# Optimization experiments

Measured on AMD Instinct MI355X. Metric: run time of the kernel, lower is better.

Reference implementation:

```python
import jax, jax.numpy as jnp
import numpy as np
import math

B, T, IN_DIM = 2, 2048, 512
D, NH, MULT, N_LAYER = 512, 8, 4, 3
N = D * MULT // NH  # per-head latent dim = 256
OUT_DIM = 512
THETA = 2 ** 16


def get_freqs(n):
    t = jnp.arange(n, dtype=jnp.float32)
    q = jnp.floor(t / 2.0) * 2.0  # quantize(q=2)
    return 1.0 / (THETA ** (q / n)) / (2.0 * math.pi)


def ln(x, eps=1e-5):
    mu = jnp.mean(x, axis=-1, keepdims=True)
    var = jnp.var(x, axis=-1, keepdims=True)
    return (x - mu) * jax.lax.rsqrt(var + eps)


def rope(phases, v):
    # phases: [T, N] broadcastable to v [B, nh, T, N]
    p = (phases % 1.0) * (2.0 * math.pi)
    pc, ps = jnp.cos(p), jnp.sin(p)
    # interleave rotate: out[..., 2i] = -v[..., 2i+1], out[..., 2i+1] = v[..., 2i]
    v_rot = jnp.stack((-v[..., 1::2], v[..., ::2]), axis=-1).reshape(v.shape)
    return v * pc + v_rot * ps


def setup_inputs() -> dict:
    key = jax.random.key(0)
    ks = jax.random.split(key, 8)
    std = 0.02
    return {
        "x": jax.random.normal(ks[0], (B, T, IN_DIM), dtype=jnp.float32),
        "w_in": jax.random.normal(ks[1], (IN_DIM, D), dtype=jnp.float32) * std,
        "b_in": jnp.zeros((D,), dtype=jnp.float32),
        "encoder": jax.random.normal(ks[2], (NH, D, N), dtype=jnp.float32) * std,
        "encoder_v": jax.random.normal(ks[3], (NH, D, N), dtype=jnp.float32) * std,
        "decoder": jax.random.normal(ks[4], (NH * N, D), dtype=jnp.float32) * std,
        "head_w": jax.random.normal(ks[5], (D, OUT_DIM), dtype=jnp.float32) * std,
        "head_b": jnp.zeros((OUT_DIM,), dtype=jnp.float32),
    }


def reference(x, w_in, b_in, encoder, encoder_v, decoder, head_w, head_b):
    freqs = get_freqs(N)  # [N]
    t_idx = jnp.arange(T, dtype=jnp.float32)
    phases = t_idx[:, None] * freqs[None, :]  # [T, N]
    # strict lower-triangular causal mask (tril diagonal=-1)
    mask = (jnp.arange(T)[:, None] > jnp.arange(T)[None, :])  # [T, T]
    dec = decoder.reshape(NH, N, D)

    xs = ln(x @ w_in + b_in)  # [B, T, D]
    for _ in range(N_LAYER):
        x_res = xs
        x_sparse = jax.nn.relu(jnp.einsum('btd,hdn->bhtn', xs, encoder))  # [B,nh,T,N]
        QR = rope(phases, x_sparse)
        scores = jnp.einsum('bhtn,bhsn->bhts', QR, QR)
        scores = jnp.where(mask, scores, 0.0)
        yKV = jnp.einsum('bhts,bsd->bhtd', scores, xs)  # V = x (head-broadcast)
        yKV = ln(yKV)
        y_sparse = jax.nn.relu(jnp.einsum('bhtd,hdn->bhtn', yKV, encoder_v))
        xy_sparse = x_sparse * y_sparse  # dropout p=0 -> identity
        yMLP = jnp.einsum('bhtn,hnd->btd', xy_sparse, dec)
        xs = ln(x_res + ln(yMLP))
    logits = xs @ head_w + head_b
    return logits
```

## Files before the change

### kernel.cpp

```cpp
#include <hip/hip_runtime.h>
#include <math.h>

constexpr int B_  = 2;
constexpr int T_  = 2048;
constexpr int D_  = 512;
constexpr int NH_ = 8;
constexpr int NL_ = 256;
constexpr int HN_ = NH_ * NL_;
constexpr int BT_ = B_ * T_;

typedef __bf16 v8bf __attribute__((ext_vector_type(8)));
typedef float  v4f  __attribute__((ext_vector_type(4)));
typedef unsigned short us8 __attribute__((ext_vector_type(8)));
typedef unsigned short us4 __attribute__((ext_vector_type(4)));

__device__ inline unsigned short f2b(float f) {
    union { float f; unsigned u; } v{f};
    unsigned r = v.u + 0x7FFF + ((v.u >> 16) & 1);
    return (unsigned short)(r >> 16);
}
__device__ inline float b2f(unsigned short u) {
    union { unsigned u; float f; } v{(unsigned)u << 16};
    return v.f;
}

__device__ __forceinline__ void g2l16(const void* g, void* l) {
    __builtin_amdgcn_global_load_lds(
        (const __attribute__((address_space(1))) void*)g,
        (__attribute__((address_space(3))) void*)l, 16, 0, 0);
}

#define TILE_IDS                                              \
    int tid = threadIdx.x;                                    \
    int lane = tid & 63, wid = tid >> 6;                      \
    int wm = (wid & 1) * 64, wn = (wid >> 1) * 64;            \
    int ln16 = lane & 15, q = lane >> 4;                      \
    int srl = lane >> 2, scl = (lane & 3) * 8;                \
    (void)wm; (void)wn;

#define T128_STAGE(Ab, lda, Bb, ldb, k0, buf)                 \
    _Pragma("unroll")                                         \
    for (int ci = 0; ci < 4; ++ci) {                          \
        int c = wid * 4 + ci;                                 \
        if (c < 8) {                                          \
            int r = c * 16 + srl;                             \
            g2l16(Ab + (long)r * lda + (k0) + scl,            \
                  (char*)As[buf] + c * 1024);                 \
        } else {                                              \
            int r = (c - 8) * 16 + srl;                       \
            g2l16(Bb + (long)r * ldb + (k0) + scl,            \
                  (char*)Bs[buf] + (c - 8) * 1024);           \
        }                                                     \
    }

#define TILE_MFMA(Asx, Bsx)                                   \
    {                                                         \
        v8bf af[4], bfr[4];                                   \
        _Pragma("unroll")                                     \
        for (int r = 0; r < 4; ++r)                           \
            af[r] = *(const v8bf*)&Asx[wm + r * 16 + ln16][q * 8]; \
        _Pragma("unroll")                                     \
        for (int c = 0; c < 4; ++c)                           \
            bfr[c] = *(const v8bf*)&Bsx[wn + c * 16 + ln16][q * 8]; \
        _Pragma("unroll")                                     \
        for (int r = 0; r < 4; ++r)                           \
            _Pragma("unroll")                                 \
            for (int c = 0; c < 4; ++c)                       \
                acc[r][c] = __builtin_amdgcn_mfma_f32_16x16x32_bf16( \
                    af[r], bfr[c], acc[r][c], 0, 0, 0);       \
    }

template <int KS, bool RELU, bool MUL, bool BF16OUT, bool LNA>
__global__ __launch_bounds__(256) void gemm128(
    const unsigned short* __restrict__ A, int lda, long sA,
    const unsigned short* __restrict__ Bt, int ldb, long sB,
    void* __restrict__ Cv, int ldc, long sC,
    const unsigned short* __restrict__ mulp, int K,
    const float* __restrict__ muinv, const float* __restrict__ colsum) {
    constexpr int NHF = KS / 32;
    int m0 = blockIdx.y * 128, n0 = blockIdx.x * 128, z = blockIdx.z;
    __shared__ unsigned short As[2][NHF][128][32];
    __shared__ unsigned short Bs[2][NHF][128][32];
    const unsigned short* Ab = A  + (long)z * sA + (long)m0 * lda;
    const unsigned short* Bb = Bt + (long)z * sB + (long)n0 * ldb;
    TILE_IDS
    v4f acc[4][4] = {};
    auto stageK = [&](int k0, int buf) {
        #pragma unroll
        for (int h = 0; h < NHF; ++h)
            #pragma unroll
            for (int ci = 0; ci < 4; ++ci) {
                int c = wid * 4 + ci;
                if (c < 8)
                    g2l16(Ab + (long)(c * 16 + srl) * lda + k0 + h * 32 + scl,
                          (char*)As[buf][h] + c * 1024);
                else
                    g2l16(Bb + (long)((c - 8) * 16 + srl) * ldb + k0 + h * 32 +
                              scl,
                          (char*)Bs[buf][h] + (c - 8) * 1024);
            }
    };
    stageK(0, 0);
    __syncthreads();
    int cur = 0;
    for (int k0 = 0; k0 < K; k0 += KS) {
        if (k0 + KS < K) stageK(k0 + KS, cur ^ 1);
        #pragma unroll
        for (int h = 0; h < NHF; ++h)
            TILE_MFMA(As[cur][h], Bs[cur][h])
        __syncthreads();
        cur ^= 1;
    }
    float* Cf = (float*)Cv;
    unsigned short* Cb = (unsigned short*)Cv;
    long zoff = (long)z * sC;
    #pragma unroll
    for (int r = 0; r < 4; ++r)
        #pragma unroll
        for (int c = 0; c < 4; ++c)
            #pragma unroll
            for (int e = 0; e < 4; ++e) {
                int row = m0 + wm + r * 16 + q * 4 + e;
                int col = n0 + wn + c * 16 + ln16;
                float v = acc[r][c][e];
                if (LNA) {
                    float2 mi = *(const float2*)&muinv[((long)z * BT_ + row) * 2];
                    float cs = colsum[(long)z * NL_ + col];
                    v = mi.y * (v - mi.x * cs);
                }
                if (RELU) v = fmaxf(v, 0.f);
                long idx = zoff + (long)row * ldc + col;
                if (MUL) v *= b2f(mulp[idx]);
                if (BF16OUT) Cb[idx] = f2b(v);
                else         Cf[idx] = v;
            }
}

__global__ __launch_bounds__(256) void enc_rope(
    const unsigned short* __restrict__ A,
    const unsigned short* __restrict__ Bt,
    unsigned short* __restrict__ xsp,
    unsigned short* __restrict__ qrh,
    unsigned short* __restrict__ qrT) {
    int m0 = blockIdx.y * 128, n0 = blockIdx.x * 128;
    __shared__ unsigned short As[2][2][128][32];
    __shared__ unsigned short Bs[2][2][128][32];
    unsigned short (*lt)[68] = (unsigned short(*)[68])&As[0][0][0][0];
    const unsigned short* Ab = A + (long)m0 * 512;
    const unsigned short* Bb = Bt + (long)n0 * 512;
    TILE_IDS
    v4f acc[4][4] = {};
    auto stageK = [&](int k0, int buf) {
        #pragma unroll
        for (int h = 0; h < 2; ++h)
            #pragma unroll
            for (int ci = 0; ci < 4; ++ci) {
                int c = wid * 4 + ci;
                if (c < 8)
                    g2l16(Ab + (long)(c * 16 + srl) * 512 + k0 + h * 32 + scl,
                          (char*)As[buf][h] + c * 1024);
                else
                    g2l16(Bb + (long)((c - 8) * 16 + srl) * 512 + k0 + h * 32 +
                              scl,
                          (char*)Bs[buf][h] + (c - 8) * 1024);
            }
    };
    stageK(0, 0);
    __syncthreads();
    int cur = 0;
    for (int k0 = 0; k0 < 512; k0 += 64) {
        if (k0 + 64 < 512) stageK(k0 + 64, cur ^ 1);
        TILE_MFMA(As[cur][0], Bs[cur][0])
        TILE_MFMA(As[cur][1], Bs[cur][1])
        __syncthreads();
        cur ^= 1;
    }
    int bb = m0 >> 11;
    int tbase = m0 & (T_ - 1);
    #pragma unroll
    for (int half = 0; half < 2; ++half) {
        if (wm == half * 64) {
            #pragma unroll
            for (int r = 0; r < 4; ++r)
                #pragma unroll
                for (int c = 0; c < 4; ++c)
                    #pragma unroll
                    for (int e = 0; e < 4; ++e) {
                        int rl = wm + r * 16 + q * 4 + e;
                        int col = n0 + wn + c * 16 + ln16;
                        float v = fmaxf(acc[r][c][e], 0.f);
                        xsp[(long)(m0 + rl) * HN_ + col] = f2b(v);
                        int n = col & (NL_ - 1);
                        int n2 = n >> 1;
                        float fr = exp2f(-(float)n2 * 0.125f) *
                                   (float)(1.0 / (2.0 * M_PI));
                        float ph = (float)(tbase + rl) * fr;
                        ph = (ph - floorf(ph)) * (float)(2.0 * M_PI);
                        float s, cc;
                        __sincosf(ph, &s, &cc);
                        float vp = __shfl_xor(v, 1, 64);
                        float o = (n & 1) ? (v * cc + vp * s)
                                          : (v * cc - vp * s);
                        int hh = col >> 8;
                        qrh[((long)(bb * 8 + hh) * T_ + tbase + rl) * NL_ + n] =
                            f2b(o);
                        lt[wn + c * 16 + ln16][rl & 63] = f2b(o);
                    }
        }
        __syncthreads();
        {
            int nrow = tid >> 1, tseg = (tid & 1) * 32;
            int colg = n0 + nrow;
            int hh = colg >> 8, nn = colg & (NL_ - 1);
            long ob = ((long)(bb * 8 + hh) * NL_ + nn) * T_ + tbase +
                      half * 64 + tseg;
            #pragma unroll
            for (int u = 0; u < 8; ++u)
                *(us4*)&qrT[ob + u * 4] = *(const us4*)&lt[nrow][tseg + u * 4];
        }
        __syncthreads();
    }
}

__global__ __launch_bounds__(256) void ct_gemm(
    const unsigned short* __restrict__ xsT,
    const unsigned short* __restrict__ qrT,
    unsigned short* __restrict__ Ct) {
    int z = blockIdx.x, nt = blockIdx.y;
    int j = blockIdx.z >> 2, mt = blockIdx.z & 3;
    int b = z >> 3;
    const unsigned short* Ab =
        xsT + (long)b * D_ * T_ + (long)(mt * 128) * T_ + j * 128;
    const unsigned short* Bb =
        qrT + (long)z * NL_ * T_ + (long)(nt * 128) * T_ + j * 128;
    __shared__ unsigned short As[2][128][32];
    __shared__ unsigned short Bs[2][128][32];
    TILE_IDS
    v4f acc[4][4] = {};
    T128_STAGE(Ab, T_, Bb, T_, 0, 0)
    __syncthreads();
    int cur = 0;
    for (int k0 = 0; k0 < 128; k0 += 32) {
        if (k0 + 32 < 128) { T128_STAGE(Ab, T_, Bb, T_, k0 + 32, cur ^ 1) }
        TILE_MFMA(As[cur], Bs[cur])
        __syncthreads();
        cur ^= 1;
    }
    unsigned short* ob = Ct + ((long)z * 16 + j) * 512 * 256;
    #pragma unroll
    for (int r = 0; r < 4; ++r)
        #pragma unroll
        for (int c = 0; c < 4; ++c)
            #pragma unroll
            for (int e = 0; e < 4; ++e) {
                int row = mt * 128 + wm + r * 16 + q * 4 + e;
                int col = nt * 128 + wn + c * 16 + ln16;
                ob[(long)row * 256 + col] = f2b(acc[r][c][e]);
            }
}

__global__ __launch_bounds__(256) void prefix_k(unsigned short* __restrict__ Ct) {
    int z = blockIdx.x, dg = blockIdx.y;
    int d = dg * 8 + (threadIdx.x >> 5);
    int n0 = (threadIdx.x & 31) * 8;
    long base = ((long)z * 16) * 512 * 256 + (long)d * 256 + n0;
    constexpr long S = 512 * 256;
    us8 vals[16];
    #pragma unroll
    for (int i = 0; i < 16; ++i)
        vals[i] = *(const us8*)&Ct[base + (long)i * S];
    float acc[8] = {};
    #pragma unroll
    for (int i = 0; i < 16; ++i) {
        us8 o;
        #pragma unroll
        for (int e = 0; e < 8; ++e) o[e] = f2b(acc[e]);
        *(us8*)&Ct[base + (long)i * S] = o;
        #pragma unroll
        for (int e = 0; e < 8; ++e) acc[e] += b2f(vals[i][e]);
    }
}

#define SD_STAGE(k0, buf)                                     \
    _Pragma("unroll")                                         \
    for (int ci = 0; ci < 2; ++ci) {                          \
        int c = wid * 2 + ci;                                 \
        g2l16(Ab + (long)(c * 16 + srl) * NL_ + (k0) + scl,   \
              (char*)As[buf] + c * 1024);                     \
    }

__global__ __launch_bounds__(256) void sdiag(const unsigned short* __restrict__ qr,
                                             unsigned short* __restrict__ Sd) {
    int z = blockIdx.x, i = blockIdx.y;
    const unsigned short* Ab = qr + ((long)z * T_ + i * 128) * NL_;
    __shared__ unsigned short As[2][128][32];
    TILE_IDS
    v4f acc[4][4] = {};
    SD_STAGE(0, 0)
    __syncthreads();
    int cur = 0;
    for (int k0 = 0; k0 < NL_; k0 += 32) {
        if (k0 + 32 < NL_) { SD_STAGE(k0 + 32, cur ^ 1) }
        TILE_MFMA(As[cur], As[cur])
        __syncthreads();
        cur ^= 1;
    }
    unsigned short* ob = Sd + ((long)z * 16 + i) * 16384;
    #pragma unroll
    for (int r = 0; r < 4; ++r)
        #pragma unroll
        for (int c = 0; c < 4; ++c)
            #pragma unroll
            for (int e = 0; e < 4; ++e) {
                int row = wm + r * 16 + q * 4 + e;
                int col = wn + c * 16 + ln16;
                float v = acc[r][c][e];
                if (row <= col) v = 0.f;
                ob[row * 128 + col] = f2b(v);
            }
}

__global__ __launch_bounds__(256) void pxg(
    const unsigned short* __restrict__ qr,
    const unsigned short* __restrict__ Pt,
    const unsigned short* __restrict__ Sd,
    const unsigned short* __restrict__ xsT,
    unsigned short* __restrict__ ykvu,
    float* __restrict__ part) {
    int z = blockIdx.x, i = blockIdx.y, nt = blockIdx.z;
    int b = z >> 3, h = z & 7;
    int n0 = nt * 128;
    const unsigned short* A1 = qr + ((long)z * T_ + i * 128) * NL_;
    const unsigned short* B1 =
        Pt + ((long)z * 16 + i) * 512 * 256 + (long)n0 * 256;
    const unsigned short* A2 = Sd + ((long)z * 16 + i) * 16384;
    const unsigned short* B2 =
        xsT + (long)b * D_ * T_ + (long)n0 * T_ + i * 128;
    __shared__ unsigned short As[2][128][32];
    __shared__ unsigned short Bs[2][128][32];
    __shared__ float sred[128][2][2];
    TILE_IDS
    v4f acc[4][4] = {};
    auto stage = [&](int s) {
        const unsigned short* Ap;
        const unsigned short* Bp;
        long lda, ldb;
        int k0;
        if (s < 8) { Ap = A1; lda = NL_; Bp = B1; ldb = 256; k0 = s * 32; }
        else       { Ap = A2; lda = 128; Bp = B2; ldb = T_;  k0 = (s - 8) * 32; }
        int bi = s & 1;
        #pragma unroll
        for (int ci = 0; ci < 4; ++ci) {
            int c = wid * 4 + ci;
            if (c < 8)
                g2l16(Ap + (long)(c * 16 + srl) * lda + k0 + scl,
                      (char*)As[bi] + c * 1024);
            else
                g2l16(Bp + (long)((c - 8) * 16 + srl) * ldb + k0 + scl,
                      (char*)Bs[bi] + (c - 8) * 1024);
        }
    };
    stage(0);
    __syncthreads();
    for (int s = 0; s < 12; ++s) {
        if (s < 11) stage(s + 1);
        int bi = s & 1;
        TILE_MFMA(As[bi], Bs[bi])
        __syncthreads();
    }
    long obase = ((long)h * BT_ + (long)b * T_ + i * 128) * D_ + n0;
    #pragma unroll
    for (int r = 0; r < 4; ++r) {
        float s1[4] = {}, s2[4] = {};
        #pragma unroll
        for (int c = 0; c < 4; ++c)
            #pragma unroll
            for (int e = 0; e < 4; ++e) {
                float v = acc[r][c][e];
                s1[e] += v;
                s2[e] += v * v;
                int rl = wm + r * 16 + q * 4 + e;
                int col = wn + c * 16 + ln16;
                ykvu[obase + (long)rl * D_ + col] = f2b(v);
            }
        #pragma unroll
        for (int e = 0; e < 4; ++e) {
            #pragma unroll
            for (int off = 1; off < 16; off <<= 1) {
                s1[e] += __shfl_xor(s1[e], off, 64);
                s2[e] += __shfl_xor(s2[e], off, 64);
            }
            if (ln16 == 0) {
                int rl = wm + r * 16 + q * 4 + e;
                sred[rl][wid >> 1][0] = s1[e];
                sred[rl][wid >> 1][1] = s2[e];
            }
        }
    }
    __syncthreads();
    if (tid < 128) {
        float a = sred[tid][0][0] + sred[tid][1][0];
        float sq = sred[tid][0][1] + sred[tid][1][1];
        long pb = ((((long)z * 16 + i) * 4 + nt) * 128 + tid) * 2;
        part[pb] = a;
        part[pb + 1] = sq;
    }
}

__global__ __launch_bounds__(128) void lnstats(const float* __restrict__ part,
                                               float* __restrict__ muinv) {
    int z = blockIdx.x, i = blockIdx.y, t = threadIdx.x;
    long pb = ((((long)z * 16 + i) * 4) * 128 + t) * 2;
    float s1 = part[pb] + part[pb + 256] + part[pb + 512] + part[pb + 768];
    float s2 = part[pb + 1] + part[pb + 257] + part[pb + 513] + part[pb + 769];
    float mu = s1 * (1.0f / 512.0f);
    float var = s2 * (1.0f / 512.0f) - mu * mu;
    float inv = rsqrtf(var + 1e-5f);
    int b = z >> 3, h = z & 7;
    long row = (long)h * BT_ + (long)b * T_ + i * 128 + t;
    muinv[row * 2]     = mu;
    muinv[row * 2 + 1] = inv;
}

__global__ __launch_bounds__(256) void colsum_k(
    const unsigned short* __restrict__ encvT, float* __restrict__ cs) {
    int lane = threadIdx.x & 63, wv = threadIdx.x >> 6;
    int g = blockIdx.x * 4 + wv;
    us8 v = *(const us8*)&encvT[(long)g * 512 + lane * 8];
    float s = 0.f;
    #pragma unroll
    for (int e = 0; e < 8; ++e) s += b2f(v[e]);
    #pragma unroll
    for (int off = 1; off < 64; off <<= 1) s += __shfl_xor(s, off, 64);
    if (lane == 0) cs[g] = s;
}

__global__ __launch_bounds__(256) void trans_cast(
    const float* __restrict__ in, long sIn, unsigned short* __restrict__ out,
    long sOut, int R, int Cc) {
    __shared__ float tl[32][33];
    int z = blockIdx.z;
    int r0 = blockIdx.y * 32, c0 = blockIdx.x * 32;
    int tx = threadIdx.x & 31, ty = threadIdx.x >> 5;
    const float* ip = in + (long)z * sIn;
    unsigned short* op = out + (long)z * sOut;
    #pragma unroll
    for (int j = 0; j < 4; ++j)
        tl[ty + j * 8][tx] = ip[(long)(r0 + ty + j * 8) * Cc + c0 + tx];
    __syncthreads();
    #pragma unroll
    for (int j = 0; j < 4; ++j)
        op[(long)(c0 + ty + j * 8) * R + r0 + tx] = f2b(tl[tx][ty + j * 8]);
}

__global__ __launch_bounds__(256) void cast_b(const float* __restrict__ in,
                                              unsigned short* __restrict__ out) {
    long i = ((long)blockIdx.x * 256 + threadIdx.x) * 4;
    float4 v = *(const float4*)&in[i];
    ushort4 o;
    o.x = f2b(v.x); o.y = f2b(v.y); o.z = f2b(v.z); o.w = f2b(v.w);
    *(ushort4*)&out[i] = o;
}

__global__ __launch_bounds__(256) void add_out4(const float* __restrict__ t,
                                                long slice,
                                                const float* __restrict__ bias,
                                                float* __restrict__ o) {
    long i = ((long)blockIdx.x * 256 + threadIdx.x) * 4;
    float4 v0 = *(const float4*)&t[i];
    float4 v1 = *(const float4*)&t[i + slice];
    float4 v2 = *(const float4*)&t[i + 2 * slice];
    float4 v3 = *(const float4*)&t[i + 3 * slice];
    float4 bv = *(const float4*)&bias[i & 511];
    float4 r;
    r.x = v0.x + v1.x + v2.x + v3.x + bv.x;
    r.y = v0.y + v1.y + v2.y + v3.y + bv.y;
    r.z = v0.z + v1.z + v2.z + v3.z + bv.z;
    r.w = v0.w + v1.w + v2.w + v3.w + bv.w;
    *(float4*)&o[i] = r;
}

__device__ inline float2 block_reduce2(float a, float b) {
    __shared__ float sa[4], sb[4];
    #pragma unroll
    for (int off = 32; off; off >>= 1) {
        a += __shfl_down(a, off, 64);
        b += __shfl_down(b, off, 64);
    }
    __syncthreads();
    int w = threadIdx.x >> 6;
    if ((threadIdx.x & 63) == 0) { sa[w] = a; sb[w] = b; }
    __syncthreads();
    return make_float2(sa[0] + sa[1] + sa[2] + sa[3],
                       sb[0] + sb[1] + sb[2] + sb[3]);
}
__device__ inline float2 ln_pair(float2 v) {
    float2 s = block_reduce2(v.x + v.y, 0.f);
    float mu = s.x * (1.0f / 512.0f);
    float dx = v.x - mu, dy = v.y - mu;
    float2 q = block_reduce2(dx * dx + dy * dy, 0.f);
    float inv = rsqrtf(q.x * (1.0f / 512.0f) + 1e-5f);
    return make_float2(dx * inv, dy * inv);
}

__global__ __launch_bounds__(256) void ln_dual4(const float* __restrict__ t,
                                                long slice,
                                                const float* __restrict__ bias,
                                                float* __restrict__ outf,
                                                unsigned short* __restrict__ outb) {
    long row = blockIdx.x;
    int c = threadIdx.x * 2;
    long i = row * 512 + c;
    float2 v0 = *(const float2*)&t[i];
    float2 v1 = *(const float2*)&t[i + slice];
    float2 v2 = *(const float2*)&t[i + 2 * slice];
    float2 v3 = *(const float2*)&t[i + 3 * slice];
    float2 bv = *(const float2*)&bias[c];
    float2 v = make_float2(v0.x + v1.x + v2.x + v3.x + bv.x,
                           v0.y + v1.y + v2.y + v3.y + bv.y);
    float2 o = ln_pair(v);
    *(float2*)&outf[i] = o;
    ushort2 ob; ob.x = f2b(o.x); ob.y = f2b(o.y);
    *(ushort2*)&outb[i] = ob;
}

__global__ __launch_bounds__(256) void combine_dual4(
    const float* __restrict__ t, long slice, const float* __restrict__ xres,
    float* __restrict__ outf, unsigned short* __restrict__ outb) {
    long row = blockIdx.x;
    int c = threadIdx.x * 2;
    long i = row * 512 + c;
    float2 v0 = *(const float2*)&t[i];
    float2 v1 = *(const float2*)&t[i + slice];
    float2 v2 = *(const float2*)&t[i + 2 * slice];
    float2 v3 = *(const float2*)&t[i + 3 * slice];
    float2 y = make_float2(v0.x + v1.x + v2.x + v3.x,
                           v0.y + v1.y + v2.y + v3.y);
    float2 l = ln_pair(y);
    float2 r = *(const float2*)&xres[i];
    float2 z = make_float2(r.x + l.x, r.y + l.y);
    float2 o = ln_pair(z);
    *(float2*)&outf[i] = o;
    ushort2 ob; ob.x = f2b(o.x); ob.y = f2b(o.y);
    *(ushort2*)&outb[i] = ob;
}

extern "C" void kernel_launch(void* const* d_in, const int* in_sizes, int n_in,
                              void* d_out, int out_size, void* d_ws,
                              size_t ws_size, hipStream_t stream) {
    const float* x      = (const float*)d_in[0];
    const float* w_in   = (const float*)d_in[1];
    const float* b_in   = (const float*)d_in[2];
    const float* enc    = (const float*)d_in[3];
    const float* enc_v  = (const float*)d_in[4];
    const float* dec    = (const float*)d_in[5];
    const float* head_w = (const float*)d_in[6];
    const float* head_b = (const float*)d_in[7];
    float* out = (float*)d_out;

    char* w = (char*)d_ws;
    auto alloc = [&](size_t bytes) { void* p = (void*)w; w += bytes; return p; };
    unsigned short* w_inT = (unsigned short*)alloc((size_t)512 * 512 * 2);
    unsigned short* headT = (unsigned short*)alloc((size_t)512 * 512 * 2);
    unsigned short* encT  = (unsigned short*)alloc((size_t)NH_ * NL_ * D_ * 2);
    unsigned short* encvT = (unsigned short*)alloc((size_t)NH_ * NL_ * D_ * 2);
    unsigned short* decT  = (unsigned short*)alloc((size_t)D_ * HN_ * 2);
    unsigned short* xb    = (unsigned short*)alloc((size_t)BT_ * D_ * 2);
    float*          tmp   = (float*)alloc((size_t)4 * BT_ * D_ * 4);
    float*          xsf0  = (float*)alloc((size_t)BT_ * D_ * 4);
    float*          xsf1  = (float*)alloc((size_t)BT_ * D_ * 4);
    unsigned short* xs_b  = (unsigned short*)alloc((size_t)BT_ * D_ * 2);
    unsigned short* xsT   = (unsigned short*)alloc((size_t)B_ * D_ * T_ * 2);
    unsigned short* xsp   = (unsigned short*)alloc((size_t)BT_ * HN_ * 2);
    unsigned short* qrh   = (unsigned short*)alloc((size_t)BT_ * HN_ * 2);
    unsigned short* qrT   = (unsigned short*)alloc((size_t)BT_ * HN_ * 2);
    unsigned short* Ct    = (unsigned short*)alloc((size_t)256 * 512 * 256 * 2);
    unsigned short* Sd    = (unsigned short*)alloc((size_t)256 * 128 * 128 * 2);
    unsigned short* ykv   = (unsigned short*)alloc((size_t)NH_ * BT_ * D_ * 2);
    float*          part  = (float*)alloc((size_t)256 * 4 * 128 * 2 * 4);
    float*          muinv = (float*)alloc((size_t)NH_ * BT_ * 2 * 4);
    float*          csum  = (float*)alloc((size_t)HN_ * 4);
    const long SL = (long)BT_ * D_;

    cast_b<<<BT_ * D_ / 1024, 256, 0, stream>>>(x, xb);
    trans_cast<<<dim3(16, 16, 1), 256, 0, stream>>>(w_in, 0, w_inT, 0, 512, 512);
    trans_cast<<<dim3(16, 16, 1), 256, 0, stream>>>(head_w, 0, headT, 0, 512, 512);
    trans_cast<<<dim3(8, 16, 8), 256, 0, stream>>>(enc, (long)D_ * NL_, encT,
                                                   (long)NL_ * D_, D_, NL_);
    trans_cast<<<dim3(8, 16, 8), 256, 0, stream>>>(enc_v, (long)D_ * NL_, encvT,
                                                   (long)NL_ * D_, D_, NL_);
    trans_cast<<<dim3(16, 64, 1), 256, 0, stream>>>(dec, 0, decT, 0, HN_, D_);
    colsum_k<<<HN_ / 4, 256, 0, stream>>>(encvT, csum);

    gemm128<64, false, false, false, false>
        <<<dim3(4, 32, 4), 256, 0, stream>>>(xb, D_, 128, w_inT, D_, 128, tmp,
                                             D_, SL, nullptr, 128, nullptr,
                                             nullptr);
    ln_dual4<<<BT_, 256, 0, stream>>>(tmp, SL, b_in, xsf0, xs_b);
    trans_cast<<<dim3(16, 64, 2), 256, 0, stream>>>(xsf0, (long)T_ * D_, xsT,
                                                    (long)D_ * T_, T_, D_);

    float* xin = xsf0;
    float* xout = xsf1;
    for (int l = 0; l < 3; ++l) {
        enc_rope<<<dim3(16, 32), 256, 0, stream>>>(xs_b, encT, xsp, qrh, qrT);
        ct_gemm<<<dim3(16, 2, 64), 256, 0, stream>>>(xsT, qrT, Ct);
        prefix_k<<<dim3(16, 64), 256, 0, stream>>>(Ct);
        sdiag<<<dim3(16, 16), 256, 0, stream>>>(qrh, Sd);
        pxg<<<dim3(16, 16, 4), 256, 0, stream>>>(qrh, Ct, Sd, xsT, ykv, part);
        lnstats<<<dim3(16, 16), 128, 0, stream>>>(part, muinv);
        gemm128<64, true, true, true, true>
            <<<dim3(2, 32, 8), 256, 0, stream>>>(
                ykv, D_, (long)BT_ * D_, encvT, D_, (long)NL_ * D_, xsp, HN_,
                NL_, xsp, 512, muinv, csum);
        gemm128<64, false, false, false, false>
            <<<dim3(4, 32, 4), 256, 0, stream>>>(
                xsp, HN_, 512, decT, HN_, 512, tmp, D_, SL, nullptr, 512,
                nullptr, nullptr);
        combine_dual4<<<BT_, 256, 0, stream>>>(tmp, SL, xin, xout, xs_b);
        trans_cast<<<dim3(16, 64, 2), 256, 0, stream>>>(xout, (long)T_ * D_,
                                                        xsT, (long)D_ * T_, T_,
                                                        D_);
        float* t = xin; xin = xout; xout = t;
    }

    gemm128<64, false, false, false, false>
        <<<dim3(4, 32, 4), 256, 0, stream>>>(xs_b, D_, 128, headT, D_, 128, tmp,
                                             D_, SL, nullptr, 128, nullptr,
                                             nullptr);
    add_out4<<<BT_ * 512 / 1024, 256, 0, stream>>>(tmp, SL, head_b, out);
}
```

Before: 627.5 us.

## Double causal chunk size from 128 to 256 in chunked linear attention

Result: faster. 588.7 us (-6.2%).

```diff
diff --git a/kernel.cpp b/kernel.cpp
--- a/kernel.cpp
+++ b/kernel.cpp
@@ -230,9 +230,9 @@
     int j = blockIdx.z >> 2, mt = blockIdx.z & 3;
     int b = z >> 3;
     const unsigned short* Ab =
-        xsT + (long)b * D_ * T_ + (long)(mt * 128) * T_ + j * 128;
+        xsT + (long)b * D_ * T_ + (long)(mt * 128) * T_ + j * 256;
     const unsigned short* Bb =
-        qrT + (long)z * NL_ * T_ + (long)(nt * 128) * T_ + j * 128;
+        qrT + (long)z * NL_ * T_ + (long)(nt * 128) * T_ + j * 256;
     __shared__ unsigned short As[2][128][32];
     __shared__ unsigned short Bs[2][128][32];
     TILE_IDS
@@ -240,13 +240,13 @@
     T128_STAGE(Ab, T_, Bb, T_, 0, 0)
     __syncthreads();
     int cur = 0;
-    for (int k0 = 0; k0 < 128; k0 += 32) {
-        if (k0 + 32 < 128) { T128_STAGE(Ab, T_, Bb, T_, k0 + 32, cur ^ 1) }
+    for (int k0 = 0; k0 < 256; k0 += 32) {
+        if (k0 + 32 < 256) { T128_STAGE(Ab, T_, Bb, T_, k0 + 32, cur ^ 1) }
         TILE_MFMA(As[cur], Bs[cur])
         __syncthreads();
         cur ^= 1;
     }
-    unsigned short* ob = Ct + ((long)z * 16 + j) * 512 * 256;
+    unsigned short* ob = Ct + ((long)z * 8 + j) * 512 * 256;
     #pragma unroll
     for (int r = 0; r < 4; ++r)
         #pragma unroll
@@ -263,15 +263,15 @@
     int z = blockIdx.x, dg = blockIdx.y;
     int d = dg * 8 + (threadIdx.x >> 5);
     int n0 = (threadIdx.x & 31) * 8;
-    long base = ((long)z * 16) * 512 * 256 + (long)d * 256 + n0;
+    long base = ((long)z * 8) * 512 * 256 + (long)d * 256 + n0;
     constexpr long S = 512 * 256;
-    us8 vals[16];
-    #pragma unroll
-    for (int i = 0; i < 16; ++i)
+    us8 vals[8];
+    #pragma unroll
+    for (int i = 0; i < 8; ++i)
         vals[i] = *(const us8*)&Ct[base + (long)i * S];
     float acc[8] = {};
     #pragma unroll
-    for (int i = 0; i < 16; ++i) {
+    for (int i = 0; i < 8; ++i) {
         us8 o;
         #pragma unroll
         for (int e = 0; e < 8; ++e) o[e] = f2b(acc[e]);
@@ -281,31 +281,41 @@
     }
 }
 
-#define SD_STAGE(k0, buf)                                     \
-    _Pragma("unroll")                                         \
-    for (int ci = 0; ci < 2; ++ci) {                          \
-        int c = wid * 2 + ci;                                 \
-        g2l16(Ab + (long)(c * 16 + srl) * NL_ + (k0) + scl,   \
-              (char*)As[buf] + c * 1024);                     \
-    }
-
 __global__ __launch_bounds__(256) void sdiag(const unsigned short* __restrict__ qr,
                                              unsigned short* __restrict__ Sd) {
-    int z = blockIdx.x, i = blockIdx.y;
-    const unsigned short* Ab = qr + ((long)z * T_ + i * 128) * NL_;
+    int z = blockIdx.x, i = blockIdx.y, qq = blockIdx.z;
+    int qm = (qq + 1) >> 1, qn = qq >> 1;
+    const unsigned short* Ab =
+        qr + ((long)z * T_ + i * 256 + qm * 128) * NL_;
+    const unsigned short* Bb =
+        qr + ((long)z * T_ + i * 256 + qn * 128) * NL_;
+    bool dual = (qm != qn);
     __shared__ unsigned short As[2][128][32];
+    __shared__ unsigned short Bs[2][128][32];
     TILE_IDS
     v4f acc[4][4] = {};
-    SD_STAGE(0, 0)
+    auto stg = [&](int k0, int buf) {
+        #pragma unroll
+        for (int ci = 0; ci < 2; ++ci) {
+            int c = wid * 2 + ci;
+            g2l16(Ab + (long)(c * 16 + srl) * NL_ + k0 + scl,
+                  (char*)As[buf] + c * 1024);
+            if (dual)
+                g2l16(Bb + (long)(c * 16 + srl) * NL_ + k0 + scl,
+                      (char*)Bs[buf] + c * 1024);
+        }
+    };
+    stg(0, 0);
     __syncthreads();
     int cur = 0;
     for (int k0 = 0; k0 < NL_; k0 += 32) {
-        if (k0 + 32 < NL_) { SD_STAGE(k0 + 32, cur ^ 1) }
-        TILE_MFMA(As[cur], As[cur])
+        if (k0 + 32 < NL_) stg(k0 + 32, cur ^ 1);
+        if (dual) { TILE_MFMA(As[cur], Bs[cur]) }
+        else      { TILE_MFMA(As[cur], As[cur]) }
         __syncthreads();
         cur ^= 1;
     }
-    unsigned short* ob = Sd + ((long)z * 16 + i) * 16384;
+    unsigned short* ob = Sd + ((long)z * 8 + i) * 65536;
     #pragma unroll
     for (int r = 0; r < 4; ++r)
         #pragma unroll
@@ -315,8 +325,8 @@
                 int row = wm + r * 16 + q * 4 + e;
                 int col = wn + c * 16 + ln16;
                 float v = acc[r][c][e];
-                if (row <= col) v = 0.f;
-                ob[row * 128 + col] = f2b(v);
+                if (!dual && row <= col) v = 0.f;
+                ob[(qm * 128 + row) * 256 + qn * 128 + col] = f2b(v);
             }
 }
 
@@ -330,24 +340,27 @@
     int z = blockIdx.x, i = blockIdx.y, nt = blockIdx.z;
     int b = z >> 3, h = z & 7;
     int n0 = nt * 128;
+    int i256 = i >> 1, hf2 = i & 1;
     const unsigned short* A1 = qr + ((long)z * T_ + i * 128) * NL_;
     const unsigned short* B1 =
-        Pt + ((long)z * 16 + i) * 512 * 256 + (long)n0 * 256;
-    const unsigned short* A2 = Sd + ((long)z * 16 + i) * 16384;
+        Pt + ((long)z * 8 + i256) * 512 * 256 + (long)n0 * 256;
+    const unsigned short* A2 = Sd + ((long)z * 8 + i256) * 65536 +
+                               (long)hf2 * 128 * 256;
     const unsigned short* B2 =
-        xsT + (long)b * D_ * T_ + (long)n0 * T_ + i * 128;
+        xsT + (long)b * D_ * T_ + (long)n0 * T_ + i256 * 256;
     __shared__ unsigned short As[2][128][32];
     __shared__ unsigned short Bs[2][128][32];
     __shared__ float sred[128][2][2];
     TILE_IDS
     v4f acc[4][4] = {};
+    int NS = 12 + hf2 * 4;
     auto stage = [&](int s) {
         const unsigned short* Ap;
         const unsigned short* Bp;
         long lda, ldb;
         int k0;
         if (s < 8) { Ap = A1; lda = NL_; Bp = B1; ldb = 256; k0 = s * 32; }
-        else       { Ap = A2; lda = 128; Bp = B2; ldb = T_;  k0 = (s - 8) * 32; }
+        else       { Ap = A2; lda = 256; Bp = B2; ldb = T_;  k0 = (s - 8) * 32; }
         int bi = s & 1;
         #pragma unroll
         for (int ci = 0; ci < 4; ++ci) {
@@ -362,8 +375,8 @@
     };
     stage(0);
     __syncthreads();
-    for (int s = 0; s < 12; ++s) {
-        if (s < 11) stage(s + 1);
+    for (int s = 0; s < NS; ++s) {
+        if (s + 1 < NS) stage(s + 1);
         int bi = s & 1;
         TILE_MFMA(As[bi], Bs[bi])
         __syncthreads();
@@ -574,8 +587,8 @@
     unsigned short* xsp   = (unsigned short*)alloc((size_t)BT_ * HN_ * 2);
     unsigned short* qrh   = (unsigned short*)alloc((size_t)BT_ * HN_ * 2);
     unsigned short* qrT   = (unsigned short*)alloc((size_t)BT_ * HN_ * 2);
-    unsigned short* Ct    = (unsigned short*)alloc((size_t)256 * 512 * 256 * 2);
-    unsigned short* Sd    = (unsigned short*)alloc((size_t)256 * 128 * 128 * 2);
+    unsigned short* Ct    = (unsigned short*)alloc((size_t)128 * 512 * 256 * 2);
+    unsigned short* Sd    = (unsigned short*)alloc((size_t)128 * 256 * 256 * 2);
     unsigned short* ykv   = (unsigned short*)alloc((size_t)NH_ * BT_ * D_ * 2);
     float*          part  = (float*)alloc((size_t)256 * 4 * 128 * 2 * 4);
     float*          muinv = (float*)alloc((size_t)NH_ * BT_ * 2 * 4);
@@ -604,9 +617,9 @@
     float* xout = xsf1;
     for (int l = 0; l < 3; ++l) {
         enc_rope<<<dim3(16, 32), 256, 0, stream>>>(xs_b, encT, xsp, qrh, qrT);
-        ct_gemm<<<dim3(16, 2, 64), 256, 0, stream>>>(xsT, qrT, Ct);
+        ct_gemm<<<dim3(16, 2, 32), 256, 0, stream>>>(xsT, qrT, Ct);
         prefix_k<<<dim3(16, 64), 256, 0, stream>>>(Ct);
-        sdiag<<<dim3(16, 16), 256, 0, stream>>>(qrh, Sd);
+        sdiag<<<dim3(16, 8, 3), 256, 0, stream>>>(qrh, Sd);
         pxg<<<dim3(16, 16, 4), 256, 0, stream>>>(qrh, Ct, Sd, xsT, ykv, part);
         lnstats<<<dim3(16, 16), 128, 0, stream>>>(part, muinv);
         gemm128<64, true, true, true, true>
```
